# Performance work log

Measured on AMD Instinct MI355X. Metric: run time of the kernel, lower is better.

Reference implementation:

```python
import jax, jax.numpy as jnp
import numpy as np

H, C = 2, 128           # heads, out_channels per head
HC = H * C              # 256 concat output dim
D_IN = 256              # in_channels
D_T = 128               # time encoder out_channels
D_MSG = 128
E_DIM = D_MSG + D_T     # edge_dim = 256
N = 50000
E = 200000
MEAN_DT, STD_DT = 0.0, 1.0
SQRT_C = np.float32(np.sqrt(C))


def _time_enc(rel_t, W_t, b_t):
    # TGN TimeEncoder: cos(Linear(rel_t.view(-1,1)))  -> [E, D_T]
    return jnp.cos(rel_t[:, None] * W_t[0] + b_t)


def _seg_softmax(alpha, dst, n_dst):
    # numerically stable scatter-softmax over destination-node segments
    amax = jax.ops.segment_max(alpha, dst, num_segments=n_dst)
    amax = jnp.where(jnp.isfinite(amax), amax, 0.0)
    ex = jnp.exp(alpha - amax[dst])
    denom = jax.ops.segment_sum(ex, dst, num_segments=n_dst)
    return ex / (denom[dst] + 1e-16)


def _transformer_conv(x_src, x_dst, ei, edge_attr, Wq, bq, Wk, bk, Wv, bv, We, Ws, bs):
    n_dst = x_dst.shape[0]
    src, dst = ei[0], ei[1]
    q = (x_dst @ Wq + bq).reshape(n_dst, H, C)
    k = ((x_src @ Wk + bk)[src]).reshape(-1, H, C)      # gather per edge
    v = ((x_src @ Wv + bv)[src]).reshape(-1, H, C)
    e = (edge_attr @ We).reshape(-1, H, C)              # lin_edge (no bias)
    alpha = jnp.sum(q[dst] * (k + e), axis=-1) / SQRT_C  # [E, H]
    alpha = _seg_softmax(alpha, dst, n_dst)
    msg = (v + e) * alpha[..., None]                    # [E, H, C]
    out = jax.ops.segment_sum(msg.reshape(-1, HC), dst, num_segments=n_dst)
    return out + x_dst @ Ws + bs                        # root/skip connection


def setup_inputs() -> dict:
    key = jax.random.key(0)
    ks = jax.random.split(key, 32)
    s = 0.05
    inp = {
        'x_user': jax.random.normal(ks[0], (N, D_IN), jnp.float32),
        'x_item': jax.random.normal(ks[1], (N, D_IN), jnp.float32),
        'last_update_user': jax.random.uniform(ks[2], (N,), jnp.float32) * 100.0,
        'last_update_item': jax.random.uniform(ks[3], (N,), jnp.float32) * 100.0,
        'edge_index_a': jax.random.randint(ks[4], (2, E), 0, N, jnp.int32),
        'edge_index_b': jax.random.randint(ks[5], (2, E), 0, N, jnp.int32),
        't_a': jax.random.uniform(ks[6], (E,), jnp.float32) * 100.0 + 100.0,
        't_b': jax.random.uniform(ks[7], (E,), jnp.float32) * 100.0 + 100.0,
        'msg_a': jax.random.normal(ks[8], (E, D_MSG), jnp.float32),
        'msg_b': jax.random.normal(ks[9], (E, D_MSG), jnp.float32),
        'W_t': jax.random.normal(ks[10], (1, D_T), jnp.float32) * s,
        'b_t': jax.random.normal(ks[11], (D_T,), jnp.float32) * s,
    }
    i = 12
    for suf in ('a', 'b'):
        for nm, shape in (('Wq', (D_IN, HC)), ('bq', (HC,)), ('Wk', (D_IN, HC)), ('bk', (HC,)),
                          ('Wv', (D_IN, HC)), ('bv', (HC,)), ('We', (E_DIM, HC)),
                          ('Ws', (D_IN, HC)), ('bs', (HC,))):
            inp[f'{nm}_{suf}'] = jax.random.normal(ks[i], shape, jnp.float32) * s
            i += 1
    return inp


def reference(x_user, x_item, last_update_user, last_update_item,
              edge_index_a, edge_index_b, t_a, t_b, msg_a, msg_b, W_t, b_t,
              Wq_a, bq_a, Wk_a, bk_a, Wv_a, bv_a, We_a, Ws_a, bs_a,
              Wq_b, bq_b, Wk_b, bk_b, Wv_b, bv_b, We_b, Ws_b, bs_b):
    # edge type a: ('user','to','item');  edge type b: ('item','rev_to','user')
    rel_a = (t_a - last_update_user[edge_index_a[0]] - MEAN_DT) / STD_DT
    ea = jnp.concatenate([_time_enc(rel_a, W_t, b_t), msg_a], axis=-1)
    rel_b = (t_b - last_update_item[edge_index_b[0]] - MEAN_DT) / STD_DT
    eb = jnp.concatenate([_time_enc(rel_b, W_t, b_t), msg_b], axis=-1)
    out_item = _transformer_conv(x_user, x_item, edge_index_a, ea,
                                 Wq_a, bq_a, Wk_a, bk_a, Wv_a, bv_a, We_a, Ws_a, bs_a)
    out_user = _transformer_conv(x_item, x_user, edge_index_b, eb,
                                 Wq_b, bq_b, Wk_b, bk_b, Wv_b, bv_b, We_b, Ws_b, bs_b)
    return out_user, out_item
```

## Files before the change

kernel.cpp:

```cpp
#include <hip/hip_runtime.h>
#include <hip/hip_bf16.h>

#define N_NODES 50000
#define E_EDGES 200000
static constexpr float INV_SQRT_C = 0.08838834764831845f;

typedef __attribute__((ext_vector_type(4))) float f32x4;
typedef __attribute__((ext_vector_type(8))) short s16x8;
typedef __attribute__((ext_vector_type(4))) short s16x4;

__device__ __forceinline__ float b2f(unsigned short u) {
  union { unsigned u; float f; } x; x.u = ((unsigned)u) << 16; return x.f;
}
__device__ __forceinline__ short f2b(float f) {
  union { float f; unsigned u; } x; x.f = f;
  unsigned r = x.u + 0x7FFFu + ((x.u >> 16) & 1u);
  return (short)(r >> 16);
}

struct WPtrs { const float* w[10]; };

__global__ __launch_bounds__(256) void prep_transpose(WPtrs p, short* __restrict__ out) {
  __shared__ short T[256 * 66];
  const int wi = blockIdx.x >> 2, cq = blockIdx.x & 3;
  const float* w = p.w[wi];
  short* o = out + wi * 65536;
  const int tid = threadIdx.x;
#pragma unroll
  for (int i = 0; i < 64; ++i) {
    int flat = tid + i * 256;
    int k = flat >> 6, cc = flat & 63;
    T[k * 66 + cc] = f2b(w[k * 256 + cq * 64 + cc]);
  }
  __syncthreads();
#pragma unroll
  for (int i = 0; i < 8; ++i) {
    int flat2 = tid + i * 256;
    int g = flat2 & 3, colb = (flat2 >> 2) & 15, ks = (flat2 >> 6) & 7, ctl = flat2 >> 9;
    int ct = cq * 4 + ctl;
    s16x8 v;
#pragma unroll
    for (int j = 0; j < 8; ++j)
      v[j] = T[(ks * 32 + g * 8 + j) * 66 + ctl * 16 + colb];
    *(s16x8*)(o + (((ct * 8 + ks) * 16 + colb) * 32 + g * 8)) = v;
  }
}

struct NJobs {
  const float* X[4];
  const short* Wt[4];
  const float* bias[4];
  unsigned short* o16[4];
  float* of[4];
};

__global__ __launch_bounds__(512) void node_gemm8(NJobs jobs, int M) {
  __shared__ __align__(16) char smem[33792];
  short* As = (short*)smem;
  const int tid = threadIdx.x;
  const int l = tid & 63;
  const int w = tid >> 6;
  const int m0 = blockIdx.x * 64;
  const bool fullblk = (m0 + 64 <= M);
  const int job = blockIdx.y;
  const float* X = jobs.X[job];
  const short* Wt = jobs.Wt[job];
  const float* bias = jobs.bias[job];
  unsigned short* o16 = jobs.o16[job];
  float* of = jobs.of[job];

  if (fullblk) {
#pragma unroll
    for (int i = 0; i < 8; ++i) {
      int flat = tid + i * 512;
      int r = flat >> 6, c4 = flat & 63;
      float4 xv = *(const float4*)(X + (size_t)(m0 + r) * 256 + c4 * 4);
      s16x4 sv; sv[0] = f2b(xv.x); sv[1] = f2b(xv.y); sv[2] = f2b(xv.z); sv[3] = f2b(xv.w);
      *(s16x4*)&As[r * 264 + c4 * 4] = sv;
    }
  } else {
#pragma unroll
    for (int i = 0; i < 8; ++i) {
      int flat = tid + i * 512;
      int r = flat >> 6, c4 = flat & 63;
      float4 xv = make_float4(0.f, 0.f, 0.f, 0.f);
      if (m0 + r < M) xv = *(const float4*)(X + (size_t)(m0 + r) * 256 + c4 * 4);
      s16x4 sv; sv[0] = f2b(xv.x); sv[1] = f2b(xv.y); sv[2] = f2b(xv.z); sv[3] = f2b(xv.w);
      *(s16x4*)&As[r * 264 + c4 * 4] = sv;
    }
  }
  __syncthreads();

  const int colb = l & 15;
  const int g = l >> 4;
  const short* wbase0 = Wt + (((2 * w + 0) * 8) * 16 + colb) * 32 + g * 8;
  const short* wbase1 = Wt + (((2 * w + 1) * 8) * 16 + colb) * 32 + g * 8;

  f32x4 acc[4][2];
#pragma unroll
  for (int m = 0; m < 4; ++m) { acc[m][0] = (f32x4)(0.0f); acc[m][1] = (f32x4)(0.0f); }
#pragma unroll
  for (int ks = 0; ks < 8; ++ks) {
    s16x8 b0 = *(const s16x8*)(wbase0 + ks * 512);
    s16x8 b1 = *(const s16x8*)(wbase1 + ks * 512);
#pragma unroll
    for (int m = 0; m < 4; ++m) {
      s16x8 a = *(const s16x8*)&As[(16 * m + colb) * 264 + ks * 32 + g * 8];
      acc[m][0] = __builtin_amdgcn_mfma_f32_16x16x32_bf16(a, b0, acc[m][0], 0, 0, 0);
      acc[m][1] = __builtin_amdgcn_mfma_f32_16x16x32_bf16(a, b1, acc[m][1], 0, 0, 0);
    }
  }
  __syncthreads();

  if (of) {
    float* buf = (float*)smem;
#pragma unroll 1
    for (int half = 0; half < 2; ++half) {
#pragma unroll
      for (int j = 0; j < 2; ++j) {
        int col = (2 * w + j) * 16 + colb;
        float bv = bias[col];
#pragma unroll
        for (int mm = 0; mm < 2; ++mm) {
          int m = half * 2 + mm;
#pragma unroll
          for (int r = 0; r < 4; ++r)
            buf[(16 * mm + g * 4 + r) * 260 + col] = acc[m][j][r] + bv;
        }
      }
      __syncthreads();
#pragma unroll
      for (int i = 0; i < 4; ++i) {
        int flat = tid + i * 512;
        int row = flat >> 6, ch = flat & 63;
        int grow = m0 + half * 32 + row;
        if (fullblk || grow < M)
          *(float4*)(of + (size_t)grow * 256 + ch * 4) = *(const float4*)&buf[row * 260 + ch * 4];
      }
      __syncthreads();
    }
  } else {
    short* buf = (short*)smem;
#pragma unroll
    for (int j = 0; j < 2; ++j) {
      int col = (2 * w + j) * 16 + colb;
      float bv = bias[col];
#pragma unroll
      for (int m = 0; m < 4; ++m)
#pragma unroll
        for (int r = 0; r < 4; ++r)
          buf[(16 * m + g * 4 + r) * 264 + col] = f2b(acc[m][j][r] + bv);
    }
    __syncthreads();
#pragma unroll
    for (int i = 0; i < 4; ++i) {
      int flat = tid + i * 512;
      int row = flat >> 5, ch = flat & 31;
      if (fullblk || m0 + row < M)
        *(s16x8*)(o16 + (size_t)(m0 + row) * 256 + ch * 8) = *(const s16x8*)&buf[row * 264 + ch * 8];
    }
  }
}

__global__ __launch_bounds__(256) void csr_count2(const int* __restrict__ eia,
                                                  const int* __restrict__ eib,
                                                  int* __restrict__ counts) {
  int t = blockIdx.x * 256 + threadIdx.x;
  const int* ei = blockIdx.y ? eib : eia;
  int* c = counts + blockIdx.y * N_NODES;
  if (t < E_EDGES) atomicAdd(&c[ei[E_EDGES + t]], 1);
}

__global__ __launch_bounds__(1024) void csr_scan2(int* __restrict__ counts,
                                                  int* __restrict__ start) {
  int* cnt = counts + blockIdx.x * N_NODES;
  int* st  = start + blockIdx.x * (N_NODES + 1);
  __shared__ int wsum[16];
  __shared__ int chunk_tot;
  __shared__ int carry_s;
  const int tid = threadIdx.x, lane = tid & 63, wid = tid >> 6;
  if (tid == 0) carry_s = 0;
  __syncthreads();
  for (int base = 0; base < N_NODES; base += 1024) {
    int gi = base + tid;
    int x = (gi < N_NODES) ? cnt[gi] : 0;
    int v = x;
#pragma unroll
    for (int d = 1; d < 64; d <<= 1) {
      int t = __shfl_up(v, d);
      if (lane >= d) v += t;
    }
    if (lane == 63) wsum[wid] = v;
    __syncthreads();
    if (tid == 0) {
      int run = 0;
#pragma unroll
      for (int i = 0; i < 16; ++i) { int t = wsum[i]; wsum[i] = run; run += t; }
      chunk_tot = run;
    }
    __syncthreads();
    if (gi < N_NODES) {
      int excl = carry_s + wsum[wid] + v - x;
      st[gi] = excl;
      cnt[gi] = excl;
    }
    __syncthreads();
    if (tid == 0) carry_s += chunk_tot;
  }
  if (tid == 0) st[N_NODES] = carry_s;
}

__global__ __launch_bounds__(256) void csr_fill2(const int* __restrict__ eia,
                                                 const int* __restrict__ eib,
                                                 int* __restrict__ counts,
                                                 int* __restrict__ pos,
                                                 unsigned short* __restrict__ esrc) {
  int t = blockIdx.x * 256 + threadIdx.x;
  const int* ei = blockIdx.y ? eib : eia;
  int* cur = counts + blockIdx.y * N_NODES;
  int* ps  = pos + blockIdx.y * E_EDGES;
  unsigned short* es = esrc + (size_t)blockIdx.y * E_EDGES;
  if (t < E_EDGES) {
    int d = ei[E_EDGES + t];
    int p = atomicAdd(&cur[d], 1);
    ps[t] = p;
    es[p] = (unsigned short)ei[t];
  }
}

__global__ __launch_bounds__(512) void edge_gemm6(
    const int* __restrict__ ei, const float* __restrict__ tvec,
    const float* __restrict__ lu, const float* __restrict__ msg,
    const float* __restrict__ Wtim, const float* __restrict__ btim,
    const short* __restrict__ WeT, const int* __restrict__ pos,
    unsigned short* __restrict__ e16g)
{
  __shared__ short attr[64 * 264];
  __shared__ float rel[64];
  __shared__ int poss[64];

  const int tid = threadIdx.x;
  const int l = tid & 63;
  const int w = tid >> 6;
  const int e0 = blockIdx.x * 64;
  const int colb = l & 15;
  const int g = l >> 4;

  const float wt = Wtim[tid & 127], bt = btim[tid & 127];

  if (tid < 64) {
    rel[tid] = tvec[e0 + tid] - lu[ei[e0 + tid]];
    poss[tid] = pos[e0 + tid];
  }
#pragma unroll
  for (int i = 0; i < 4; ++i) {
    int flat = tid + i * 512;
    int row = flat >> 5, c4 = flat & 31;
    float4 mv = *(const float4*)(msg + (size_t)(e0 + row) * 128 + c4 * 4);
    s16x4 sv; sv[0] = f2b(mv.x); sv[1] = f2b(mv.y); sv[2] = f2b(mv.z); sv[3] = f2b(mv.w);
    *(s16x4*)&attr[row * 264 + 128 + c4 * 4] = sv;
  }
  __syncthreads();

  {
    int col = tid & 127;
    int r0 = (tid >> 7) * 16;
#pragma unroll
    for (int i = 0; i < 16; ++i)
      attr[(r0 + i) * 264 + col] = f2b(__cosf(rel[r0 + i] * wt + bt));
  }
  __syncthreads();

  const short* wbase0 = WeT + (((2 * w + 0) * 8) * 16 + colb) * 32 + g * 8;
  const short* wbase1 = WeT + (((2 * w + 1) * 8) * 16 + colb) * 32 + g * 8;
  f32x4 acc[4][2];
#pragma unroll
  for (int m = 0; m < 4; ++m) { acc[m][0] = (f32x4)(0.0f); acc[m][1] = (f32x4)(0.0f); }
#pragma unroll
  for (int ks = 0; ks < 8; ++ks) {
    s16x8 b0 = *(const s16x8*)(wbase0 + ks * 512);
    s16x8 b1 = *(const s16x8*)(wbase1 + ks * 512);
#pragma unroll
    for (int m = 0; m < 4; ++m) {
      s16x8 a = *(const s16x8*)&attr[(16 * m + colb) * 264 + ks * 32 + g * 8];
      acc[m][0] = __builtin_amdgcn_mfma_f32_16x16x32_bf16(a, b0, acc[m][0], 0, 0, 0);
      acc[m][1] = __builtin_amdgcn_mfma_f32_16x16x32_bf16(a, b1, acc[m][1], 0, 0, 0);
    }
  }
  __syncthreads();
#pragma unroll
  for (int j = 0; j < 2; ++j)
#pragma unroll
    for (int m = 0; m < 4; ++m)
#pragma unroll
      for (int r = 0; r < 4; ++r)
        attr[(16 * m + g * 4 + r) * 264 + (2 * w + j) * 16 + colb] = f2b(acc[m][j][r]);
  __syncthreads();

#pragma unroll
  for (int i = 0; i < 4; ++i) {
    int flat = tid + i * 512;
    int row = flat >> 5, cg = flat & 31;
    size_t slot = (size_t)poss[row];
    *(s16x8*)(e16g + slot * 256 + cg * 8) = *(const s16x8*)&attr[row * 264 + cg * 8];
  }
}

__global__ __launch_bounds__(256) void aggregate_fused5(
    const int* __restrict__ start, const unsigned short* __restrict__ esrc,
    const unsigned short* __restrict__ Q16, const unsigned short* __restrict__ K16,
    const unsigned short* __restrict__ V16, const unsigned short* __restrict__ e16,
    float* __restrict__ out)
{
  const int wave = blockIdx.x * 4 + (threadIdx.x >> 6);
  const int nwaves = gridDim.x * 4;
  const int lane = threadIdx.x & 63;
  const int c0 = lane * 4;

  for (int d = wave; d < N_NODES; d += nwaves) {
    const int s0 = start[d], s1 = start[d + 1];
    if (s1 <= s0) continue;

    s16x4 qv = *(const s16x4*)(Q16 + (size_t)d * 256 + c0);
    const float q0 = b2f((unsigned short)qv[0]), q1 = b2f((unsigned short)qv[1]);
    const float q2 = b2f((unsigned short)qv[2]), q3 = b2f((unsigned short)qv[3]);

    float den = 0.f;
    float a0 = 0.f, a1 = 0.f, a2 = 0.f, a3 = 0.f;
    int p = s0;

#define EDGE_LOAD(J, PP)                                                    \
    int s##J = (int)esrc[PP];                                               \
    s16x4 ev##J = *(const s16x4*)(e16 + (size_t)(PP) * 256 + c0);           \
    s16x4 kv##J = *(const s16x4*)(K16 + (size_t)s##J * 256 + c0);           \
    s16x4 vv##J = *(const s16x4*)(V16 + (size_t)s##J * 256 + c0);           \
    float e0##J = b2f((unsigned short)ev##J[0]), e1##J = b2f((unsigned short)ev##J[1]); \
    float e2##J = b2f((unsigned short)ev##J[2]), e3##J = b2f((unsigned short)ev##J[3]); \
    float dt##J = q0 * (b2f((unsigned short)kv##J[0]) + e0##J)              \
                + q1 * (b2f((unsigned short)kv##J[1]) + e1##J)              \
                + q2 * (b2f((unsigned short)kv##J[2]) + e2##J)              \
                + q3 * (b2f((unsigned short)kv##J[3]) + e3##J);

#define EDGE_ACC(J)                                                         \
    den += ex##J;                                                           \
    a0 += ex##J * (b2f((unsigned short)vv##J[0]) + e0##J);                  \
    a1 += ex##J * (b2f((unsigned short)vv##J[1]) + e1##J);                  \
    a2 += ex##J * (b2f((unsigned short)vv##J[2]) + e2##J);                  \
    a3 += ex##J * (b2f((unsigned short)vv##J[3]) + e3##J);

    for (; p + 4 <= s1; p += 4) {
      EDGE_LOAD(A, p)  EDGE_LOAD(B, p + 1)  EDGE_LOAD(C, p + 2)  EDGE_LOAD(D, p + 3)
      dtA += __shfl_xor(dtA, 1);  dtB += __shfl_xor(dtB, 1);
      dtC += __shfl_xor(dtC, 1);  dtD += __shfl_xor(dtD, 1);
      dtA += __shfl_xor(dtA, 2);  dtB += __shfl_xor(dtB, 2);
      dtC += __shfl_xor(dtC, 2);  dtD += __shfl_xor(dtD, 2);
      dtA += __shfl_xor(dtA, 4);  dtB += __shfl_xor(dtB, 4);
      dtC += __shfl_xor(dtC, 4);  dtD += __shfl_xor(dtD, 4);
      dtA += __shfl_xor(dtA, 8);  dtB += __shfl_xor(dtB, 8);
      dtC += __shfl_xor(dtC, 8);  dtD += __shfl_xor(dtD, 8);
      dtA += __shfl_xor(dtA, 16); dtB += __shfl_xor(dtB, 16);
      dtC += __shfl_xor(dtC, 16); dtD += __shfl_xor(dtD, 16);
      float exA = __expf(dtA * INV_SQRT_C), exB = __expf(dtB * INV_SQRT_C);
      float exC = __expf(dtC * INV_SQRT_C), exD = __expf(dtD * INV_SQRT_C);
      EDGE_ACC(A) EDGE_ACC(B) EDGE_ACC(C) EDGE_ACC(D)
    }
    for (; p < s1; ++p) {
      EDGE_LOAD(T, p)
      dtT += __shfl_xor(dtT, 1);
      dtT += __shfl_xor(dtT, 2);
      dtT += __shfl_xor(dtT, 4);
      dtT += __shfl_xor(dtT, 8);
      dtT += __shfl_xor(dtT, 16);
      float exT = __expf(dtT * INV_SQRT_C);
      EDGE_ACC(T)
    }
#undef EDGE_LOAD
#undef EDGE_ACC

    float inv = 1.f / (den + 1e-16f);
    float4* op = (float4*)(out + (size_t)d * 256 + c0);
    float4 o = *op;
    o.x += a0 * inv; o.y += a1 * inv; o.z += a2 * inv; o.w += a3 * inv;
    *op = o;
  }
}

extern "C" void kernel_launch(void* const* d_in, const int* in_sizes, int n_in,
                              void* d_out, int out_size, void* d_ws, size_t ws_size,
                              hipStream_t stream) {
  const float* x_user  = (const float*)d_in[0];
  const float* x_item  = (const float*)d_in[1];
  const float* lu_user = (const float*)d_in[2];
  const float* lu_item = (const float*)d_in[3];
  const int*   ei_a    = (const int*)d_in[4];
  const int*   ei_b    = (const int*)d_in[5];
  const float* t_a     = (const float*)d_in[6];
  const float* t_b     = (const float*)d_in[7];
  const float* msg_a   = (const float*)d_in[8];
  const float* msg_b   = (const float*)d_in[9];
  const float* W_t     = (const float*)d_in[10];
  const float* b_t     = (const float*)d_in[11];
  const float* Wq_a = (const float*)d_in[12]; const float* bq_a = (const float*)d_in[13];
  const float* Wk_a = (const float*)d_in[14]; const float* bk_a = (const float*)d_in[15];
  const float* Wv_a = (const float*)d_in[16]; const float* bv_a = (const float*)d_in[17];
  const float* We_a = (const float*)d_in[18];
  const float* Ws_a = (const float*)d_in[19]; const float* bs_a = (const float*)d_in[20];
  const float* Wq_b = (const float*)d_in[21]; const float* bq_b = (const float*)d_in[22];
  const float* Wk_b = (const float*)d_in[23]; const float* bk_b = (const float*)d_in[24];
  const float* Wv_b = (const float*)d_in[25]; const float* bv_b = (const float*)d_in[26];
  const float* We_b = (const float*)d_in[27];
  const float* Ws_b = (const float*)d_in[28]; const float* bs_b = (const float*)d_in[29];

  float* out_user = (float*)d_out;
  float* out_item = (float*)d_out + (size_t)N_NODES * 256;

  WPtrs wp;
  wp.w[0] = Wq_a; wp.w[1] = Wk_a; wp.w[2] = Wv_a; wp.w[3] = Ws_a; wp.w[4] = We_a;
  wp.w[5] = Wq_b; wp.w[6] = Wk_b; wp.w[7] = Wv_b; wp.w[8] = Ws_b; wp.w[9] = We_b;

  dim3 blk(256);
  dim3 blk512(512);
  dim3 gW(40);
  dim3 gN4((N_NODES + 63) / 64, 4);
  dim3 gE(E_EDGES / 64);
  dim3 gEt2((E_EDGES + 255) / 256, 2);
  dim3 gAgg(1024);

  char* ws = (char*)d_ws;
  size_t off = 0;
  short* WtT = (short*)(ws + off); off += (size_t)10 * 65536 * 2;
  unsigned short* Q16 = (unsigned short*)(ws + off); off += (size_t)N_NODES * 256 * 2;
  unsigned short* K16 = (unsigned short*)(ws + off); off += (size_t)N_NODES * 256 * 2;
  unsigned short* V16 = (unsigned short*)(ws + off); off += (size_t)N_NODES * 256 * 2;
  unsigned short* e16 = (unsigned short*)(ws + off); off += (size_t)E_EDGES * 256 * 2;
  int* pos    = (int*)(ws + off); off += (size_t)2 * E_EDGES * 4;
  int* counts = (int*)(ws + off); off += (size_t)2 * N_NODES * 4;
  int* startb = (int*)(ws + off); off += (size_t)2 * (N_NODES + 1) * 4;
  unsigned short* esrc = (unsigned short*)(ws + off); off += (size_t)2 * E_EDGES * 2;
  if (ws_size < off) return;

  prep_transpose<<<gW, blk, 0, stream>>>(wp, WtT);

  hipMemsetAsync(counts, 0, (size_t)2 * N_NODES * 4, stream);
  csr_count2<<<gEt2, blk, 0, stream>>>(ei_a, ei_b, counts);
  csr_scan2<<<2, 1024, 0, stream>>>(counts, startb);
  csr_fill2<<<gEt2, blk, 0, stream>>>(ei_a, ei_b, counts, pos, esrc);

  {
    NJobs ja;
    ja.X[0] = x_user; ja.X[1] = x_user; ja.X[2] = x_item; ja.X[3] = x_item;
    ja.Wt[0] = WtT + 1 * 65536; ja.Wt[1] = WtT + 2 * 65536;
    ja.Wt[2] = WtT + 0 * 65536; ja.Wt[3] = WtT + 3 * 65536;
    ja.bias[0] = bk_a; ja.bias[1] = bv_a; ja.bias[2] = bq_a; ja.bias[3] = bs_a;
    ja.o16[0] = K16; ja.o16[1] = V16; ja.o16[2] = Q16; ja.o16[3] = nullptr;
    ja.of[0] = nullptr; ja.of[1] = nullptr; ja.of[2] = nullptr; ja.of[3] = out_item;
    node_gemm8<<<gN4, blk512, 0, stream>>>(ja, N_NODES);
  }
  edge_gemm6<<<gE, blk512, 0, stream>>>(ei_a, t_a, lu_user, msg_a, W_t, b_t,
      WtT + 4 * 65536, pos, e16);
  aggregate_fused5<<<gAgg, blk, 0, stream>>>(startb, esrc, Q16, K16, V16, e16, out_item);

  {
    NJobs jb;
    jb.X[0] = x_item; jb.X[1] = x_item; jb.X[2] = x_user; jb.X[3] = x_user;
    jb.Wt[0] = WtT + 6 * 65536; jb.Wt[1] = WtT + 7 * 65536;
    jb.Wt[2] = WtT + 5 * 65536; jb.Wt[3] = WtT + 8 * 65536;
    jb.bias[0] = bk_b; jb.bias[1] = bv_b; jb.bias[2] = bq_b; jb.bias[3] = bs_b;
    jb.o16[0] = K16; jb.o16[1] = V16; jb.o16[2] = Q16; jb.o16[3] = nullptr;
    jb.of[0] = nullptr; jb.of[1] = nullptr; jb.of[2] = nullptr; jb.of[3] = out_user;
    node_gemm8<<<gN4, blk512, 0, stream>>>(jb, N_NODES);
  }
  edge_gemm6<<<gE, blk512, 0, stream>>>(ei_b, t_b, lu_item, msg_b, W_t, b_t,
      WtT + 9 * 65536, pos + E_EDGES, e16);
  aggregate_fused5<<<gAgg, blk, 0, stream>>>(startb + (N_NODES + 1), esrc + E_EDGES,
      Q16, K16, V16, e16, out_user);
}
```

Baseline: 594.5 us.

## Fuse node and edge GEMMs into one interleaved launch; pre-convert x to bf16

Merges the node projection GEMM and the edge-attribute GEMM into a single kernel whose blocks alternate between node tiles and edge tiles, so compute-bound and memory-bound work share the device and one launch per edge type is removed. Also adds a pass that converts x_user/x_item to bf16 once, so each of the four node GEMM jobs reads half-size inputs instead of re-converting fp32. The extra conversion pass and its workspace cost more memory traffic up front, and it falls back to fp32 inputs when the workspace is too small.

```diff
diff --git a/kernel.cpp b/kernel.cpp
--- a/kernel.cpp
+++ b/kernel.cpp
@@ -4,6 +4,10 @@
 #define N_NODES 50000
 #define E_EDGES 200000
 static constexpr float INV_SQRT_C = 0.08838834764831845f;
+static constexpr int NB_NODE = ((N_NODES + 63) / 64) * 4;
+static constexpr int NB_EDGE = E_EDGES / 64;
+static constexpr int NB_PAIR = 2 * NB_EDGE;
+static constexpr int NB_FUSED = NB_NODE + NB_EDGE;
 
 typedef __attribute__((ext_vector_type(4))) float f32x4;
 typedef __attribute__((ext_vector_type(8))) short s16x8;
@@ -46,120 +50,19 @@
   }
 }
 
-struct NJobs {
-  const float* X[4];
-  const short* Wt[4];
-  const float* bias[4];
-  unsigned short* o16[4];
-  float* of[4];
-};
-
-__global__ __launch_bounds__(512) void node_gemm8(NJobs jobs, int M) {
-  __shared__ __align__(16) char smem[33792];
-  short* As = (short*)smem;
-  const int tid = threadIdx.x;
-  const int l = tid & 63;
-  const int w = tid >> 6;
-  const int m0 = blockIdx.x * 64;
-  const bool fullblk = (m0 + 64 <= M);
-  const int job = blockIdx.y;
-  const float* X = jobs.X[job];
-  const short* Wt = jobs.Wt[job];
-  const float* bias = jobs.bias[job];
-  unsigned short* o16 = jobs.o16[job];
-  float* of = jobs.of[job];
-
-  if (fullblk) {
-#pragma unroll
-    for (int i = 0; i < 8; ++i) {
-      int flat = tid + i * 512;
-      int r = flat >> 6, c4 = flat & 63;
-      float4 xv = *(const float4*)(X + (size_t)(m0 + r) * 256 + c4 * 4);
-      s16x4 sv; sv[0] = f2b(xv.x); sv[1] = f2b(xv.y); sv[2] = f2b(xv.z); sv[3] = f2b(xv.w);
-      *(s16x4*)&As[r * 264 + c4 * 4] = sv;
-    }
-  } else {
-#pragma unroll
-    for (int i = 0; i < 8; ++i) {
-      int flat = tid + i * 512;
-      int r = flat >> 6, c4 = flat & 63;
-      float4 xv = make_float4(0.f, 0.f, 0.f, 0.f);
-      if (m0 + r < M) xv = *(const float4*)(X + (size_t)(m0 + r) * 256 + c4 * 4);
-      s16x4 sv; sv[0] = f2b(xv.x); sv[1] = f2b(xv.y); sv[2] = f2b(xv.z); sv[3] = f2b(xv.w);
-      *(s16x4*)&As[r * 264 + c4 * 4] = sv;
-    }
-  }
-  __syncthreads();
-
-  const int colb = l & 15;
-  const int g = l >> 4;
-  const short* wbase0 = Wt + (((2 * w + 0) * 8) * 16 + colb) * 32 + g * 8;
-  const short* wbase1 = Wt + (((2 * w + 1) * 8) * 16 + colb) * 32 + g * 8;
-
-  f32x4 acc[4][2];
-#pragma unroll
-  for (int m = 0; m < 4; ++m) { acc[m][0] = (f32x4)(0.0f); acc[m][1] = (f32x4)(0.0f); }
-#pragma unroll
-  for (int ks = 0; ks < 8; ++ks) {
-    s16x8 b0 = *(const s16x8*)(wbase0 + ks * 512);
-    s16x8 b1 = *(const s16x8*)(wbase1 + ks * 512);
-#pragma unroll
-    for (int m = 0; m < 4; ++m) {
-      s16x8 a = *(const s16x8*)&As[(16 * m + colb) * 264 + ks * 32 + g * 8];
-      acc[m][0] = __builtin_amdgcn_mfma_f32_16x16x32_bf16(a, b0, acc[m][0], 0, 0, 0);
-      acc[m][1] = __builtin_amdgcn_mfma_f32_16x16x32_bf16(a, b1, acc[m][1], 0, 0, 0);
-    }
-  }
-  __syncthreads();
-
-  if (of) {
-    float* buf = (float*)smem;
-#pragma unroll 1
-    for (int half = 0; half < 2; ++half) {
-#pragma unroll
-      for (int j = 0; j < 2; ++j) {
-        int col = (2 * w + j) * 16 + colb;
-        float bv = bias[col];
-#pragma unroll
-        for (int mm = 0; mm < 2; ++mm) {
-          int m = half * 2 + mm;
-#pragma unroll
-          for (int r = 0; r < 4; ++r)
-            buf[(16 * mm + g * 4 + r) * 260 + col] = acc[m][j][r] + bv;
-        }
-      }
-      __syncthreads();
-#pragma unroll
-      for (int i = 0; i < 4; ++i) {
-        int flat = tid + i * 512;
-        int row = flat >> 6, ch = flat & 63;
-        int grow = m0 + half * 32 + row;
-        if (fullblk || grow < M)
-          *(float4*)(of + (size_t)grow * 256 + ch * 4) = *(const float4*)&buf[row * 260 + ch * 4];
-      }
-      __syncthreads();
-    }
-  } else {
-    short* buf = (short*)smem;
-#pragma unroll
-    for (int j = 0; j < 2; ++j) {
-      int col = (2 * w + j) * 16 + colb;
-      float bv = bias[col];
-#pragma unroll
-      for (int m = 0; m < 4; ++m)
-#pragma unroll
-        for (int r = 0; r < 4; ++r)
-          buf[(16 * m + g * 4 + r) * 264 + col] = f2b(acc[m][j][r] + bv);
-    }
-    __syncthreads();
-#pragma unroll
-    for (int i = 0; i < 4; ++i) {
-      int flat = tid + i * 512;
-      int row = flat >> 5, ch = flat & 31;
-      if (fullblk || m0 + row < M)
-        *(s16x8*)(o16 + (size_t)(m0 + row) * 256 + ch * 8) = *(const s16x8*)&buf[row * 264 + ch * 8];
-    }
-  }
+__global__ __launch_bounds__(256) void conv_x(const float* __restrict__ xu,
+                                              const float* __restrict__ xi,
+                                              unsigned short* __restrict__ x16u,
+                                              unsigned short* __restrict__ x16i) {
+  const float* in = blockIdx.y ? xi : xu;
+  unsigned short* out = blockIdx.y ? x16i : x16u;
+  size_t base = ((size_t)blockIdx.x * 256 + threadIdx.x) * 8;
+  float4 a = *(const float4*)(in + base);
+  float4 b = *(const float4*)(in + base + 4);
+  s16x8 v;
+  v[0] = f2b(a.x); v[1] = f2b(a.y); v[2] = f2b(a.z); v[3] = f2b(a.w);
+  v[4] = f2b(b.x); v[5] = f2b(b.y); v[6] = f2b(b.z); v[7] = f2b(b.w);
+  *(s16x8*)(out + base) = v;
 }
 
 __global__ __launch_bounds__(256) void csr_count2(const int* __restrict__ eia,
@@ -228,81 +131,206 @@
   }
 }
 
-__global__ __launch_bounds__(512) void edge_gemm6(
-    const int* __restrict__ ei, const float* __restrict__ tvec,
-    const float* __restrict__ lu, const float* __restrict__ msg,
-    const float* __restrict__ Wtim, const float* __restrict__ btim,
-    const short* __restrict__ WeT, const int* __restrict__ pos,
-    unsigned short* __restrict__ e16g)
-{
-  __shared__ short attr[64 * 264];
-  __shared__ float rel[64];
-  __shared__ int poss[64];
-
+struct FusedArgs {
+  const unsigned short* X16[4];
+  const float* Xf[4];
+  const short* Wt[4];
+  const float* bias[4];
+  unsigned short* o16[4];
+  float* of[4];
+  int use16;
+  const int* ei; const float* tvec; const float* lu; const float* msg;
+  const float* Wtim; const float* btim; const short* WeT; const int* pos;
+  unsigned short* e16g;
+};
+
+__global__ __launch_bounds__(512) void fused_ne(FusedArgs A) {
+  __shared__ __align__(16) char smem[34816];
+  const int bx = blockIdx.x;
   const int tid = threadIdx.x;
   const int l = tid & 63;
   const int w = tid >> 6;
-  const int e0 = blockIdx.x * 64;
   const int colb = l & 15;
   const int g = l >> 4;
 
-  const float wt = Wtim[tid & 127], bt = btim[tid & 127];
-
-  if (tid < 64) {
-    rel[tid] = tvec[e0 + tid] - lu[ei[e0 + tid]];
-    poss[tid] = pos[e0 + tid];
-  }
-#pragma unroll
-  for (int i = 0; i < 4; ++i) {
-    int flat = tid + i * 512;
-    int row = flat >> 5, c4 = flat & 31;
-    float4 mv = *(const float4*)(msg + (size_t)(e0 + row) * 128 + c4 * 4);
-    s16x4 sv; sv[0] = f2b(mv.x); sv[1] = f2b(mv.y); sv[2] = f2b(mv.z); sv[3] = f2b(mv.w);
-    *(s16x4*)&attr[row * 264 + 128 + c4 * 4] = sv;
-  }
-  __syncthreads();
-
-  {
-    int col = tid & 127;
-    int r0 = (tid >> 7) * 16;
-#pragma unroll
-    for (int i = 0; i < 16; ++i)
-      attr[(r0 + i) * 264 + col] = f2b(__cosf(rel[r0 + i] * wt + bt));
-  }
-  __syncthreads();
-
-  const short* wbase0 = WeT + (((2 * w + 0) * 8) * 16 + colb) * 32 + g * 8;
-  const short* wbase1 = WeT + (((2 * w + 1) * 8) * 16 + colb) * 32 + g * 8;
-  f32x4 acc[4][2];
-#pragma unroll
-  for (int m = 0; m < 4; ++m) { acc[m][0] = (f32x4)(0.0f); acc[m][1] = (f32x4)(0.0f); }
-#pragma unroll
-  for (int ks = 0; ks < 8; ++ks) {
-    s16x8 b0 = *(const s16x8*)(wbase0 + ks * 512);
-    s16x8 b1 = *(const s16x8*)(wbase1 + ks * 512);
-#pragma unroll
-    for (int m = 0; m < 4; ++m) {
-      s16x8 a = *(const s16x8*)&attr[(16 * m + colb) * 264 + ks * 32 + g * 8];
-      acc[m][0] = __builtin_amdgcn_mfma_f32_16x16x32_bf16(a, b0, acc[m][0], 0, 0, 0);
-      acc[m][1] = __builtin_amdgcn_mfma_f32_16x16x32_bf16(a, b1, acc[m][1], 0, 0, 0);
-    }
-  }
-  __syncthreads();
-#pragma unroll
-  for (int j = 0; j < 2; ++j)
-#pragma unroll
-    for (int m = 0; m < 4; ++m)
-#pragma unroll
-      for (int r = 0; r < 4; ++r)
-        attr[(16 * m + g * 4 + r) * 264 + (2 * w + j) * 16 + colb] = f2b(acc[m][j][r]);
-  __syncthreads();
-
-#pragma unroll
-  for (int i = 0; i < 4; ++i) {
-    int flat = tid + i * 512;
-    int row = flat >> 5, cg = flat & 31;
-    size_t slot = (size_t)poss[row];
-    *(s16x8*)(e16g + slot * 256 + cg * 8) = *(const s16x8*)&attr[row * 264 + cg * 8];
+  int nb = -1, eb = -1;
+  if (bx < NB_PAIR) { if (bx & 1) eb = bx >> 1; else nb = bx >> 1; }
+  else nb = NB_EDGE + (bx - NB_PAIR);
+
+  if (nb >= 0) {
+    short* As = (short*)smem;
+    const int job = nb / 782;
+    const int m0 = (nb - job * 782) * 64;
+    const bool fullblk = (m0 + 64 <= N_NODES);
+    const short* Wt = A.Wt[job];
+    const float* bias = A.bias[job];
+    unsigned short* o16 = A.o16[job];
+    float* of = A.of[job];
+
+    if (A.use16) {
+      const unsigned short* X = A.X16[job];
+      if (fullblk) {
+#pragma unroll
+        for (int i = 0; i < 4; ++i) {
+          int flat = tid + i * 512;
+          int r = flat >> 5, cg = flat & 31;
+          *(s16x8*)&As[r * 264 + cg * 8] = *(const s16x8*)(X + (size_t)(m0 + r) * 256 + cg * 8);
+        }
+      } else {
+#pragma unroll
+        for (int i = 0; i < 4; ++i) {
+          int flat = tid + i * 512;
+          int r = flat >> 5, cg = flat & 31;
+          s16x8 v = (s16x8)(short)0;
+          if (m0 + r < N_NODES) v = *(const s16x8*)(X + (size_t)(m0 + r) * 256 + cg * 8);
+          *(s16x8*)&As[r * 264 + cg * 8] = v;
+        }
+      }
+    } else {
+      const float* X = A.Xf[job];
+#pragma unroll
+      for (int i = 0; i < 8; ++i) {
+        int flat = tid + i * 512;
+        int r = flat >> 6, c4 = flat & 63;
+        float4 xv = make_float4(0.f, 0.f, 0.f, 0.f);
+        if (fullblk || m0 + r < N_NODES) xv = *(const float4*)(X + (size_t)(m0 + r) * 256 + c4 * 4);
+        s16x4 sv; sv[0] = f2b(xv.x); sv[1] = f2b(xv.y); sv[2] = f2b(xv.z); sv[3] = f2b(xv.w);
+        *(s16x4*)&As[r * 264 + c4 * 4] = sv;
+      }
+    }
+    __syncthreads();
+
+    const short* wbase0 = Wt + (((2 * w + 0) * 8) * 16 + colb) * 32 + g * 8;
+    const short* wbase1 = Wt + (((2 * w + 1) * 8) * 16 + colb) * 32 + g * 8;
+
+    f32x4 acc[4][2];
+#pragma unroll
+    for (int m = 0; m < 4; ++m) { acc[m][0] = (f32x4)(0.0f); acc[m][1] = (f32x4)(0.0f); }
+#pragma unroll
+    for (int ks = 0; ks < 8; ++ks) {
+      s16x8 b0 = *(const s16x8*)(wbase0 + ks * 512);
+      s16x8 b1 = *(const s16x8*)(wbase1 + ks * 512);
+#pragma unroll
+      for (int m = 0; m < 4; ++m) {
+        s16x8 a = *(const s16x8*)&As[(16 * m + colb) * 264 + ks * 32 + g * 8];
+        acc[m][0] = __builtin_amdgcn_mfma_f32_16x16x32_bf16(a, b0, acc[m][0], 0, 0, 0);
+        acc[m][1] = __builtin_amdgcn_mfma_f32_16x16x32_bf16(a, b1, acc[m][1], 0, 0, 0);
+      }
+    }
+    __syncthreads();
+
+    if (of) {
+      float* buf = (float*)smem;
+#pragma unroll 1
+      for (int half = 0; half < 2; ++half) {
+#pragma unroll
+        for (int j = 0; j < 2; ++j) {
+          int col = (2 * w + j) * 16 + colb;
+          float bv = bias[col];
+#pragma unroll
+          for (int mm = 0; mm < 2; ++mm) {
+            int m = half * 2 + mm;
+#pragma unroll
+            for (int r = 0; r < 4; ++r)
+              buf[(16 * mm + g * 4 + r) * 260 + col] = acc[m][j][r] + bv;
+          }
+        }
+        __syncthreads();
+#pragma unroll
+        for (int i = 0; i < 4; ++i) {
+          int flat = tid + i * 512;
+          int row = flat >> 6, ch = flat & 63;
+          int grow = m0 + half * 32 + row;
+          if (fullblk || grow < N_NODES)
+            *(float4*)(of + (size_t)grow * 256 + ch * 4) = *(const float4*)&buf[row * 260 + ch * 4];
+        }
+        __syncthreads();
+      }
+    } else {
+      short* buf = (short*)smem;
+#pragma unroll
+      for (int j = 0; j < 2; ++j) {
+        int col = (2 * w + j) * 16 + colb;
+        float bv = bias[col];
+#pragma unroll
+        for (int m = 0; m < 4; ++m)
+#pragma unroll
+          for (int r = 0; r < 4; ++r)
+            buf[(16 * m + g * 4 + r) * 264 + col] = f2b(acc[m][j][r] + bv);
+      }
+      __syncthreads();
+#pragma unroll
+      for (int i = 0; i < 4; ++i) {
+        int flat = tid + i * 512;
+        int row = flat >> 5, ch = flat & 31;
+        if (fullblk || m0 + row < N_NODES)
+          *(s16x8*)(o16 + (size_t)(m0 + row) * 256 + ch * 8) = *(const s16x8*)&buf[row * 264 + ch * 8];
+      }
+    }
+  } else {
+    short* attr = (short*)smem;
+    float* rel  = (float*)(smem + 33792);
+    int*   poss = (int*)(smem + 34048);
+    const int e0 = eb * 64;
+
+    const float wt = A.Wtim[tid & 127], bt = A.btim[tid & 127];
+
+    if (tid < 64) {
+      rel[tid] = A.tvec[e0 + tid] - A.lu[A.ei[e0 + tid]];
+      poss[tid] = A.pos[e0 + tid];
+    }
+#pragma unroll
+    for (int i = 0; i < 4; ++i) {
+      int flat = tid + i * 512;
+      int row = flat >> 5, c4 = flat & 31;
+      float4 mv = *(const float4*)(A.msg + (size_t)(e0 + row) * 128 + c4 * 4);
+      s16x4 sv; sv[0] = f2b(mv.x); sv[1] = f2b(mv.y); sv[2] = f2b(mv.z); sv[3] = f2b(mv.w);
+      *(s16x4*)&attr[row * 264 + 128 + c4 * 4] = sv;
+    }
+    __syncthreads();
+
+    {
+      int col = tid & 127;
+      int r0 = (tid >> 7) * 16;
+#pragma unroll
+      for (int i = 0; i < 16; ++i)
+        attr[(r0 + i) * 264 + col] = f2b(__cosf(rel[r0 + i] * wt + bt));
+    }
+    __syncthreads();
+
+    const short* wbase0 = A.WeT + (((2 * w + 0) * 8) * 16 + colb) * 32 + g * 8;
+    const short* wbase1 = A.WeT + (((2 * w + 1) * 8) * 16 + colb) * 32 + g * 8;
+    f32x4 acc[4][2];
+#pragma unroll
+    for (int m = 0; m < 4; ++m) { acc[m][0] = (f32x4)(0.0f); acc[m][1] = (f32x4)(0.0f); }
+#pragma unroll
+    for (int ks = 0; ks < 8; ++ks) {
+      s16x8 b0 = *(const s16x8*)(wbase0 + ks * 512);
+      s16x8 b1 = *(const s16x8*)(wbase1 + ks * 512);
+#pragma unroll
+      for (int m = 0; m < 4; ++m) {
+        s16x8 a = *(const s16x8*)&attr[(16 * m + colb) * 264 + ks * 32 + g * 8];
+        acc[m][0] = __builtin_amdgcn_mfma_f32_16x16x32_bf16(a, b0, acc[m][0], 0, 0, 0);
+        acc[m][1] = __builtin_amdgcn_mfma_f32_16x16x32_bf16(a, b1, acc[m][1], 0, 0, 0);
+      }
+    }
+    __syncthreads();
+#pragma unroll
+    for (int j = 0; j < 2; ++j)
+#pragma unroll
+      for (int m = 0; m < 4; ++m)
+#pragma unroll
+        for (int r = 0; r < 4; ++r)
+          attr[(16 * m + g * 4 + r) * 264 + (2 * w + j) * 16 + colb] = f2b(acc[m][j][r]);
+    __syncthreads();
+
+#pragma unroll
+    for (int i = 0; i < 4; ++i) {
+      int flat = tid + i * 512;
+      int row = flat >> 5, cg = flat & 31;
+      size_t slot = (size_t)poss[row];
+      *(s16x8*)(A.e16g + slot * 256 + cg * 8) = *(const s16x8*)&attr[row * 264 + cg * 8];
+    }
   }
 }
 
@@ -421,10 +449,10 @@
   dim3 blk(256);
   dim3 blk512(512);
   dim3 gW(40);
-  dim3 gN4((N_NODES + 63) / 64, 4);
-  dim3 gE(E_EDGES / 64);
+  dim3 gF(NB_FUSED);
   dim3 gEt2((E_EDGES + 255) / 256, 2);
   dim3 gAgg(1024);
+  dim3 gCv(6250, 2);
 
   char* ws = (char*)d_ws;
   size_t off = 0;
@@ -437,7 +465,11 @@
   int* counts = (int*)(ws + off); off += (size_t)2 * N_NODES * 4;
   int* startb = (int*)(ws + off); off += (size_t)2 * (N_NODES + 1) * 4;
   unsigned short* esrc = (unsigned short*)(ws + off); off += (size_t)2 * E_EDGES * 2;
-  if (ws_size < off) return;
+  const size_t off_base = off;
+  unsigned short* X16u = (unsigned short*)(ws + off); off += (size_t)N_NODES * 256 * 2;
+  unsigned short* X16i = (unsigned short*)(ws + off); off += (size_t)N_NODES * 256 * 2;
+  const bool use_x16 = (ws_size >= off);
+  if (!use_x16 && ws_size < off_base) return;
 
   prep_transpose<<<gW, blk, 0, stream>>>(wp, WtT);
 
@@ -446,32 +478,41 @@
   csr_scan2<<<2, 1024, 0, stream>>>(counts, startb);
   csr_fill2<<<gEt2, blk, 0, stream>>>(ei_a, ei_b, counts, pos, esrc);
 
+  if (use_x16)
+    conv_x<<<gCv, blk, 0, stream>>>(x_user, x_item, X16u, X16i);
+
   {
-    NJobs ja;
-    ja.X[0] = x_user; ja.X[1] = x_user; ja.X[2] = x_item; ja.X[3] = x_item;
-    ja.Wt[0] = WtT + 1 * 65536; ja.Wt[1] = WtT + 2 * 65536;
-    ja.Wt[2] = WtT + 0 * 65536; ja.Wt[3] = WtT + 3 * 65536;
-    ja.bias[0] = bk_a; ja.bias[1] = bv_a; ja.bias[2] = bq_a; ja.bias[3] = bs_a;
-    ja.o16[0] = K16; ja.o16[1] = V16; ja.o16[2] = Q16; ja.o16[3] = nullptr;
-    ja.of[0] = nullptr; ja.of[1] = nullptr; ja.of[2] = nullptr; ja.of[3] = out_item;
-    node_gemm8<<<gN4, blk512, 0, stream>>>(ja, N_NODES);
-  }
-  edge_gemm6<<<gE, blk512, 0, stream>>>(ei_a, t_a, lu_user, msg_a, W_t, b_t,
-      WtT + 4 * 65536, pos, e16);
+    FusedArgs Aa;
+    Aa.X16[0] = X16u; Aa.X16[1] = X16u; Aa.X16[2] = X16i; Aa.X16[3] = X16i;
+    Aa.Xf[0] = x_user; Aa.Xf[1] = x_user; Aa.Xf[2] = x_item; Aa.Xf[3] = x_item;
+    Aa.Wt[0] = WtT + 1 * 65536; Aa.Wt[1] = WtT + 2 * 65536;
+    Aa.Wt[2] = WtT + 0 * 65536; Aa.Wt[3] = WtT + 3 * 65536;
+    Aa.bias[0] = bk_a; Aa.bias[1] = bv_a; Aa.bias[2] = bq_a; Aa.bias[3] = bs_a;
+    Aa.o16[0] = K16; Aa.o16[1] = V16; Aa.o16[2] = Q16; Aa.o16[3] = nullptr;
+    Aa.of[0] = nullptr; Aa.of[1] = nullptr; Aa.of[2] = nullptr; Aa.of[3] = out_item;
+    Aa.use16 = use_x16 ? 1 : 0;
+    Aa.ei = ei_a; Aa.tvec = t_a; Aa.lu = lu_user; Aa.msg = msg_a;
+    Aa.Wtim = W_t; Aa.btim = b_t; Aa.WeT = WtT + 4 * 65536; Aa.pos = pos;
+    Aa.e16g = e16;
+    fused_ne<<<gF, blk512, 0, stream>>>(Aa);
+  }
   aggregate_fused5<<<gAgg, blk, 0, stream>>>(startb, esrc, Q16, K16, V16, e16, out_item);
 
   {
-    NJobs jb;
-    jb.X[0] = x_item; jb.X[1] = x_item; jb.X[2] = x_user; jb.X[3] = x_user;
-    jb.Wt[0] = WtT + 6 * 65536; jb.Wt[1] = WtT + 7 * 65536;
-    jb.Wt[2] = WtT + 5 * 65536; jb.Wt[3] = WtT + 8 * 65536;
-    jb.bias[0] = bk_b; jb.bias[1] = bv_b; jb.bias[2] = bq_b; jb.bias[3] = bs_b;
-    jb.o16[0] = K16; jb.o16[1] = V16; jb.o16[2] = Q16; jb.o16[3] = nullptr;
-    jb.of[0] = nullptr; jb.of[1] = nullptr; jb.of[2] = nullptr; jb.of[3] = out_user;
-    node_gemm8<<<gN4, blk512, 0, stream>>>(jb, N_NODES);
-  }
-  edge_gemm6<<<gE, blk512, 0, stream>>>(ei_b, t_b, lu_item, msg_b, W_t, b_t,
-      WtT + 9 * 65536, pos + E_EDGES, e16);
+    FusedArgs Ab;
+    Ab.X16[0] = X16i; Ab.X16[1] = X16i; Ab.X16[2] = X16u; Ab.X16[3] = X16u;
+    Ab.Xf[0] = x_item; Ab.Xf[1] = x_item; Ab.Xf[2] = x_user; Ab.Xf[3] = x_user;
+    Ab.Wt[0] = WtT + 6 * 65536; Ab.Wt[1] = WtT + 7 * 65536;
+    Ab.Wt[2] = WtT + 5 * 65536; Ab.Wt[3] = WtT + 8 * 65536;
+    Ab.bias[0] = bk_b; Ab.bias[1] = bv_b; Ab.bias[2] = bq_b; Ab.bias[3] = bs_b;
+    Ab.o16[0] = K16; Ab.o16[1] = V16; Ab.o16[2] = Q16; Ab.o16[3] = nullptr;
+    Ab.of[0] = nullptr; Ab.of[1] = nullptr; Ab.of[2] = nullptr; Ab.of[3] = out_user;
+    Ab.use16 = use_x16 ? 1 : 0;
+    Ab.ei = ei_b; Ab.tvec = t_b; Ab.lu = lu_item; Ab.msg = msg_b;
+    Ab.Wtim = W_t; Ab.btim = b_t; Ab.WeT = WtT + 9 * 65536; Ab.pos = pos + E_EDGES;
+    Ab.e16g = e16;
+    fused_ne<<<gF, blk512, 0, stream>>>(Ab);
+  }
   aggregate_fused5<<<gAgg, blk, 0, stream>>>(startb + (N_NODES + 1), esrc + E_EDGES,
       Q16, K16, V16, e16, out_user);
 }
```

After: 587.0 us. About the same (-1.3%).
